# Kernel tuning notes

Hardware: AMD Instinct MI355X
Metric: run time of the kernel (lower is better)

## Reference

```python
import jax, jax.numpy as jnp
import numpy as np

N_SEGMENT = 8   # frames per clip (init arg n_segment)
P = 4           # patch_size (init arg)
EPS = 1e-5      # torch F.layer_norm default eps


def setup_inputs() -> dict:
    key = jax.random.key(0)
    # (b*t, c, h, w) = (16*8, 256, 28, 28)
    x = jax.random.normal(key, (128, 256, 28, 28), dtype=jnp.float32)
    return {"x": x}


def _layer_norm(x):
    # F.layer_norm over last dim, no affine params
    m = jnp.mean(x, axis=-1, keepdims=True)
    v = jnp.var(x, axis=-1, keepdims=True)
    return (x - m) * jax.lax.rsqrt(v + EPS)


def _self_attention(x):
    # q = k = v = x; scores = softmax(q k^T / sqrt(E)); out = scores @ v
    e = x.shape[-1]
    scores = jnp.einsum('bqe,bke->bqk', x, x) * (1.0 / float(np.sqrt(e)))
    scores = jax.nn.softmax(scores, axis=-1)
    return jnp.einsum('bqk,bke->bqe', scores, x)


def reference(x):
    t, p = N_SEGMENT, P
    bt, c, h, w = x.shape
    b = bt // t
    ph, pw = h // p, w // p
    e = p * p * c  # patch embedding dim = 4096

    # rearrange '(b t) c (ph p1) (pw p2) -> (b ph pw) t (p1 p2 c)'
    y = x.reshape(b, t, c, ph, p, pw, p)
    y = y.transpose(0, 3, 5, 1, 4, 6, 2).reshape(b * ph * pw, t, e)

    # temporal: layernorm + shift-left-diff + self-attention + residual
    xn = _layer_norm(y)
    xn = jnp.concatenate([xn[:, 1:], jnp.zeros_like(xn[:, :1])], axis=1) - xn
    y = _self_attention(xn) + y

    # rearrange '(b ph pw) t e -> (b t) (ph pw) e'
    y = y.reshape(b, ph, pw, t, e).transpose(0, 3, 1, 2, 4).reshape(b * t, ph * pw, e)

    # spatial: layernorm + self-attention + residual
    xn = _layer_norm(y)
    y = _self_attention(xn) + y

    # rearrange '(b t) (ph pw) (p1 p2 c) -> (b t) c (ph p1) (pw p2)'
    y = y.reshape(b, t, ph, pw, p, p, c)
    y = y.transpose(0, 1, 6, 2, 4, 3, 5).reshape(bt, c, h, w)
    return y
```

## Files before the change

### kernel.cpp

```cpp
#include <hip/hip_runtime.h>


#define IDX36(a,b) ((((a)*8)+(b))-((((a)*((a)+1)))/2))

typedef __attribute__((ext_vector_type(8)))  short bf16x8;
typedef __attribute__((ext_vector_type(16))) float f32x16;

__device__ __forceinline__ float wsum64(float v){
  #pragma unroll
  for (int off=32; off; off>>=1) v += __shfl_xor(v, off);
  return v;
}
__device__ __forceinline__ float wsum32(float v){
  #pragma unroll
  for (int off=16; off; off>>=1) v += __shfl_xor(v, off);
  return v;
}
__device__ __forceinline__ unsigned int rne_bf16(float f){
  unsigned int b = __float_as_uint(f);
  return (b + 0x7FFFu + ((b>>16)&1u)) >> 16;
}

__global__ __launch_bounds__(256) void k_t1(const float* __restrict__ x, float* __restrict__ wsG){
  const int bx = blockIdx.x;
  const int b = bx / 112;
  const int ph = (bx % 112) / 16;
  const int slice = bx & 15;
  const int c0 = slice * 16;
  const int tid = threadIdx.x;

  __shared__ float lds[8*16*116];
  const float4* x4 = reinterpret_cast<const float4*>(x);

  #pragma unroll
  for (int t=0;t<8;t++){
    const int base = ((b*8+t)*256 + c0)*196 + ph*28;
    {
      const int f = tid, c = f/28, m = f%28;
      *reinterpret_cast<float4*>(&lds[(t*16+c)*116 + m*4]) = x4[base + c*196 + m];
    }
    if (tid < 192){
      const int f = 256+tid, c = f/28, m = f%28;
      *reinterpret_cast<float4*>(&lds[(t*16+c)*116 + m*4]) = x4[base + c*196 + m];
    }
  }
  __syncthreads();

  const int pw   = tid >> 5;
  const int slot = tid & 31;
  const int c    = slot >> 1;
  const int p1b  = (slot & 1) * 2;

  float v[8][8];
  #pragma unroll
  for (int t=0;t<8;t++){
    const float* p = &lds[(t*16+c)*116 + p1b*28 + pw*4];
    const float4 a  = *reinterpret_cast<const float4*>(p);
    const float4 b2 = *reinterpret_cast<const float4*>(p + 28);
    v[t][0]=a.x;  v[t][1]=a.y;  v[t][2]=a.z;  v[t][3]=a.w;
    v[t][4]=b2.x; v[t][5]=b2.y; v[t][6]=b2.z; v[t][7]=b2.w;
  }

  float Au[36], sm[8];
  #pragma unroll
  for (int a2=0;a2<8;a2++){
    float s0 = 0.f;
    #pragma unroll
    for (int e=0;e<8;e++) s0 += v[a2][e];
    sm[a2] = s0;
    #pragma unroll
    for (int b2=a2;b2<8;b2++){
      float s = 0.f;
      #pragma unroll
      for (int e=0;e<8;e++) s += v[a2][e]*v[b2][e];
      Au[IDX36(a2,b2)] = s;
    }
  }
  #pragma unroll
  for (int i=0;i<36;i++) Au[i] = wsum32(Au[i]);
  #pragma unroll
  for (int t=0;t<8;t++) sm[t] = wsum32(sm[t]);

  if (slot == 0 && pw < 7){
    const int base = ((b*49 + ph*7 + pw)*16 + slice)*44;
    #pragma unroll
    for (int i=0;i<36;i++) wsG[base+i] = Au[i];
    #pragma unroll
    for (int t=0;t<8;t++)  wsG[base+36+t] = sm[t];
  }
}

__global__ __launch_bounds__(64) void k_t2(const float* __restrict__ wsG, float* __restrict__ wsWt){
  const int seq = blockIdx.x;
  const int lane = threadIdx.x;
  __shared__ float red[44];
  if (lane < 44){
    float a = 0.f;
    #pragma unroll
    for (int s=0;s<16;s++) a += wsG[(seq*16+s)*44 + lane];
    red[lane] = a;
  }
  __syncthreads();
  if (lane < 8){
    const int i = lane;
    float Ar[36], mean[8], rstd[8];
    #pragma unroll
    for (int k=0;k<36;k++) Ar[k] = red[k];
    #pragma unroll
    for (int t=0;t<8;t++){
      const float sv = red[36+t];
      mean[t] = sv * (1.f/4096.f);
      const float var = Ar[IDX36(t,t)] * (1.f/4096.f) - mean[t]*mean[t];
      rstd[t] = rsqrtf(var + 1e-5f);
    }
    #define GV(a,b) ((((a)<8)&&((b)<8)) ? (rstd[(a)]*rstd[(b)]*(Ar[((a)<=(b))?IDX36((a),(b)):IDX36((b),(a))] - 4096.f*mean[(a)]*mean[(b)])) : 0.f)
    float l[8]; float mx = -1e30f;
    #pragma unroll
    for (int j=0;j<8;j++){
      const float sij = GV(i+1,j+1) - GV(i+1,j) - GV(i,j+1) + GV(i,j);
      l[j] = sij * (1.f/64.f);
      mx = fmaxf(mx, l[j]);
    }
    float ss = 0.f;
    #pragma unroll
    for (int j=0;j<8;j++){ l[j] = __expf(l[j]-mx); ss += l[j]; }
    const float inv = 1.f/ss;
    float cc = 0.f;
    #pragma unroll
    for (int k2=0;k2<8;k2++){
      const float q = (((k2>=1)? l[k2-1] : 0.f) - l[k2]) * inv;
      const float wv2 = q * rstd[k2];
      wsWt[seq*72 + i*8 + k2] = wv2;
      cc -= wv2 * mean[k2];
    }
    wsWt[seq*72 + 64 + i] = cc;
    #undef GV
  }
}

__global__ __launch_bounds__(256) void k_t3(const float* __restrict__ x, const float* __restrict__ wsWt,
                                            unsigned short* __restrict__ y1u){
  const int bx = blockIdx.x;
  const int b = bx / 112;
  const int ph = (bx % 112) / 16;
  const int slice = bx & 15;
  const int c0 = slice * 16;
  const int tid = threadIdx.x;

  __shared__ float Wl[7][72];
  for (int idx=tid; idx<504; idx+=256)
    Wl[idx/72][idx%72] = wsWt[(b*49 + ph*7 + idx/72)*72 + idx%72];
  __syncthreads();

  const float4* x4 = reinterpret_cast<const float4*>(x);

  #pragma unroll
  for (int fi=0; fi<2; fi++){
    const int f = fi*256 + tid;
    if (f < 448){
      const int c = f/28, m = f%28, pw = m%7, p1 = m/7;
      float4 v[8];
      #pragma unroll
      for (int t=0;t<8;t++) v[t] = x4[((b*8+t)*256 + c0+c)*196 + ph*28 + m];
      const float* W = Wl[pw];
      const int pp = ph*7 + pw;
      #pragma unroll
      for (int i=0;i<8;i++){
        const float ci = W[64+i];
        float4 o;
        o.x = v[i].x + ci; o.y = v[i].y + ci; o.z = v[i].z + ci; o.w = v[i].w + ci;
        #pragma unroll
        for (int j=0;j<8;j++){
          const float w = W[i*8+j];
          o.x += w*v[j].x; o.y += w*v[j].y; o.z += w*v[j].z; o.w += w*v[j].w;
        }
        const unsigned int h0=rne_bf16(o.x), h1=rne_bf16(o.y), h2=rne_bf16(o.z), h3=rne_bf16(o.w);
        const unsigned int l0=rne_bf16(o.x-__uint_as_float(h0<<16));
        const unsigned int l1=rne_bf16(o.y-__uint_as_float(h1<<16));
        const unsigned int l2=rne_bf16(o.z-__uint_as_float(h2<<16));
        const unsigned int l3=rne_bf16(o.w-__uint_as_float(h3<<16));
        const size_t ybase = (size_t)((b*8+i)*49 + pp)*8192 + (c0+c)*16 + p1*4;
        *reinterpret_cast<uint2*>(&y1u[ybase])        = make_uint2(h0|(h1<<16), h2|(h3<<16));
        *reinterpret_cast<uint2*>(&y1u[ybase + 4096]) = make_uint2(l0|(l1<<16), l2|(l3<<16));
      }
    }
  }
}

__global__ __launch_bounds__(256,3) void k_s1(const unsigned short* __restrict__ y1u, float* __restrict__ wsA){
  const int bt = blockIdx.x >> 2;
  const int slice = blockIdx.x & 3;
  const int tid = threadIdx.x;
  const int wave = tid >> 6, lane = tid & 63;

  __shared__ unsigned short Ah[64*136];
  __shared__ float red[64*52];
  for (int i=tid; i<64*52; i+=256) red[i] = 0.f;

  for (int idx=tid; idx<15*128; idx+=256){
    const int rr = 49 + idx/128, cc = idx%128;
    Ah[rr*136 + cc] = (rr==49) ? (unsigned short)0x3F80 : (unsigned short)0;
  }

  f32x16 acc00, acc01, acc11;
  #pragma unroll
  for (int i=0;i<16;i++){ acc00[i]=0.f; acc01[i]=0.f; acc11[i]=0.f; }

  const int r0 = lane & 31;
  const int koff = (lane >> 5) * 8;
  const int lrow = tid >> 4;
  const int lq   = tid & 15;

#define ISSUE(pf, ch) { \
  _Pragma("unroll") \
  for (int p=0;p<4;p++){ \
    const int row = p*16 + lrow; \
    pf[p] = make_uint4(0u,0u,0u,0u); \
    if (row < 49) pf[p] = *reinterpret_cast<const uint4*>(&y1u[(size_t)(bt*49+row)*8192 + slice*1024 + (ch)*128 + lq*8]); } }

#define CW(pf) { \
  _Pragma("unroll") \
  for (int p=0;p<4;p++){ \
    const int row = p*16 + lrow; \
    if (row < 49) *reinterpret_cast<uint4*>(&Ah[row*136 + lq*8]) = pf[p]; } }

#define MF() { \
  _Pragma("unroll") \
  for (int kk=0;kk<2;kk++){ \
    const int kw = (wave + kk*4)*16; \
    const bf16x8 f0 = *reinterpret_cast<const bf16x8*>(&Ah[ r0     *136 + kw + koff]); \
    const bf16x8 f1 = *reinterpret_cast<const bf16x8*>(&Ah[(32+r0)*136 + kw + koff]); \
    acc00 = __builtin_amdgcn_mfma_f32_32x32x16_bf16(f0, f0, acc00, 0,0,0); \
    acc01 = __builtin_amdgcn_mfma_f32_32x32x16_bf16(f0, f1, acc01, 0,0,0); \
    acc11 = __builtin_amdgcn_mfma_f32_32x32x16_bf16(f1, f1, acc11, 0,0,0); } }

  uint4 pfA[4], pfB[4];
  ISSUE(pfA, 0);
  #pragma unroll
  for (int ch=0; ch<8; ch+=2){
    if (ch+1<8) ISSUE(pfB, ch+1);
    __syncthreads();
    CW(pfA);
    __syncthreads();
    MF();
    if (ch+2<8) ISSUE(pfA, ch+2);
    __syncthreads();
    CW(pfB);
    __syncthreads();
    MF();
  }
  __syncthreads();

  const int ccol = lane & 31;
  const int rbase = 4*(lane>>5);
  #pragma unroll
  for (int q2=0;q2<16;q2++){
    const int rr = (q2&3) + 8*(q2>>2) + rbase;
    atomicAdd(&red[ rr    *52 + ccol     ], acc00[q2]);
    atomicAdd(&red[ rr    *52 + 32 + ccol], acc01[q2]);
    atomicAdd(&red[(rr+32)*52 + 32 + ccol], acc11[q2]);
  }
  __syncthreads();
  float* wp = wsA + blockIdx.x * 2500;
  for (int idx=tid; idx<2500; idx+=256){
    const int i2 = idx/50, j2 = idx%50;
    wp[idx] = (i2>=32 && j2<32) ? red[j2*52+i2] : red[i2*52+j2];
  }
#undef ISSUE
#undef CW
#undef MF
}

__global__ __launch_bounds__(256) void k_s2(const float* __restrict__ wsA, float* __restrict__ wsWT, float* __restrict__ wsC){
  const int bt = blockIdx.x;
  const int tid = threadIdx.x;
  __shared__ float A[2500];
  __shared__ float m[49], r[49];
  for (int idx=tid; idx<2548; idx+=256) wsWT[bt*2548+idx] = 0.f;
  for (int idx=tid; idx<2500; idx+=256){
    float v = 0.f;
    #pragma unroll
    for (int sl=0; sl<4; sl++) v += wsA[(bt*4+sl)*2500 + idx];
    A[idx] = v;
  }
  __syncthreads();
  if (tid < 49){
    const float mm = A[49*50+tid] * (1.f/4096.f);
    const float var = A[tid*50+tid] * (1.f/4096.f) - mm*mm;
    m[tid]=mm; r[tid]=rsqrtf(var+1e-5f);
  }
  __syncthreads();
  const int wv = tid>>6, lane = tid&63;
  for (int i=wv; i<49; i+=4){
    const float ri = r[i], mi = m[i];
    float rv=0.f, mv=0.f, L=-1e30f;
    if (lane < 49){
      rv = r[lane]; mv = m[lane];
      L = ri*rv*(A[i*50+lane] - 4096.f*mi*mv) * (1.f/64.f);
    }
    float mx = L;
    #pragma unroll
    for (int off=32; off; off>>=1) mx = fmaxf(mx, __shfl_xor(mx, off));
    const float p = (lane<49) ? __expf(L-mx) : 0.f;
    const float ss = wsum64(p);
    const float Wv = (p/ss)*rv;
    if (lane < 49) wsWT[bt*2548 + lane*52 + i] = Wv + ((lane==i) ? 1.f : 0.f);
    const float cp = wsum64(-Wv*mv);
    if (lane == 0) wsC[bt*49+i] = cp;
  }
}

__global__ __launch_bounds__(256,2) void k_s3(const unsigned short* __restrict__ y1u, const float* __restrict__ wsWT,
                                              const float* __restrict__ wsC, float* __restrict__ out){
  const int bt = blockIdx.x >> 2;
  const int chunk = blockIdx.x & 3;
  const int tid = threadIdx.x;
  const int wave = tid >> 6, lane = tid & 63;

  __shared__ unsigned short Wh[64*68], Wlo[64*68];
  __shared__ unsigned short Yh[4][32*68], Ylo[4][32*68];

  for (int idx=tid; idx<64*64; idx+=256){
    const int i = idx>>6, j = idx&63;
    float v = 0.f;
    if (i < 49){
      if (j < 49)       v = wsWT[bt*2548 + j*52 + i];
      else if (j == 49) v = wsC[bt*49 + i];
    }
    const unsigned int u = __float_as_uint(v);
    const float lo = v - __uint_as_float(u & 0xFFFF0000u);
    Wh [i*68+j] = (unsigned short)(u>>16);
    Wlo[i*68+j] = (unsigned short)rne_bf16(lo);
  }
  unsigned short* yh = &Yh[wave][0];
  unsigned short* yl = &Ylo[wave][0];
  for (int idx=lane; idx<32*16; idx+=64){
    const int e = idx>>4, jj = idx&15;
    if (jj > 0){
      yh[e*68 + 48 + jj] = (jj==1) ? 0x3F80 : 0;
      yl[e*68 + 48 + jj] = 0;
    }
  }
  __syncthreads();

  const int r0 = lane & 31;
  const int koff = (lane >> 5) * 8;
  bf16x8 A0h[4], A0l[4], A1h[4], A1l[4];
  #pragma unroll
  for (int kk=0;kk<4;kk++){
    const int off = kk*16 + koff;
    A0h[kk] = *reinterpret_cast<const bf16x8*>(&Wh [ r0     *68 + off]);
    A0l[kk] = *reinterpret_cast<const bf16x8*>(&Wlo[ r0     *68 + off]);
    A1h[kk] = *reinterpret_cast<const bf16x8*>(&Wh [(32+r0)*68 + off]);
    A1l[kk] = *reinterpret_cast<const bf16x8*>(&Wlo[(32+r0)*68 + off]);
  }

  const unsigned short* ybu = y1u + (size_t)bt*49*8192;
  float* ob_base = out + bt*200704;

#define S3_LOAD(pf, t) { \
  const int ecol0 = chunk*1024 + ((t)*4+wave)*32; \
  _Pragma("unroll") \
  for (int p=0;p<7;p++){ \
    const int idx = p*64 + lane; const int j = idx>>3; const int sub = idx&7; \
    pf[p] = make_uint4(0u,0u,0u,0u); \
    if (j < 49) pf[p] = *reinterpret_cast<const uint4*>(&ybu[(size_t)j*8192 + (sub>>2)*4096 + ecol0 + (sub&3)*8]); } }

#define S3_WRITE(pf) { \
  _Pragma("unroll") \
  for (int p=0;p<7;p++){ \
    const int idx = p*64 + lane; const int j = idx>>3; const int sub = idx&7; \
    if (j < 49){ \
      unsigned short* dst = (sub>>2) ? yl : yh; \
      const int e0 = (sub&3)*8; \
      const unsigned int uu[4] = {pf[p].x, pf[p].y, pf[p].z, pf[p].w}; \
      _Pragma("unroll") \
      for (int s=0;s<4;s++){ \
        dst[(e0 + s*2    )*68 + j] = (unsigned short)(uu[s] & 0xFFFFu); \
        dst[(e0 + s*2 + 1)*68 + j] = (unsigned short)(uu[s] >> 16); } } } }

  uint4 pf[7];
  S3_LOAD(pf, 0);
  S3_WRITE(pf);

  #pragma unroll
  for (int t=0;t<8;t++){
    if (t < 7) S3_LOAD(pf, t+1);

    f32x16 acc0, acc1;
    #pragma unroll
    for (int i=0;i<16;i++){ acc0[i]=0.f; acc1[i]=0.f; }

    #pragma unroll
    for (int kk=0;kk<4;kk++){
      const int off = kk*16 + koff;
      const bf16x8 Bh = *reinterpret_cast<const bf16x8*>(&yh[r0*68 + off]);
      const bf16x8 Bl = *reinterpret_cast<const bf16x8*>(&yl[r0*68 + off]);
      acc0 = __builtin_amdgcn_mfma_f32_32x32x16_bf16(A0h[kk], Bh, acc0, 0,0,0);
      acc0 = __builtin_amdgcn_mfma_f32_32x32x16_bf16(A0h[kk], Bl, acc0, 0,0,0);
      acc0 = __builtin_amdgcn_mfma_f32_32x32x16_bf16(A0l[kk], Bh, acc0, 0,0,0);
      acc1 = __builtin_amdgcn_mfma_f32_32x32x16_bf16(A1h[kk], Bh, acc1, 0,0,0);
      acc1 = __builtin_amdgcn_mfma_f32_32x32x16_bf16(A1h[kk], Bl, acc1, 0,0,0);
      acc1 = __builtin_amdgcn_mfma_f32_32x32x16_bf16(A1l[kk], Bh, acc1, 0,0,0);
    }

    {
      const int ecol = chunk*1024 + (t*4+wave)*32 + r0;
      const int c  = ecol >> 4;
      const int p1 = (ecol >> 2) & 3;
      const int p2 = ecol & 3;
      float* ob = ob_base + c*784 + p1*28 + p2;
      const int rbase = 4*(lane>>5);
      #pragma unroll
      for (int q=0;q<16;q++){
        const int i0 = (q&3) + 8*(q>>2) + rbase;
        ob[(i0/7)*112 + (i0%7)*4] = acc0[q];
        const int i1 = 32 + i0;
        if (i1 < 49) ob[(i1/7)*112 + (i1%7)*4] = acc1[q];
      }
    }

    if (t < 7) S3_WRITE(pf);
  }
#undef S3_LOAD
#undef S3_WRITE
}

extern "C" void kernel_launch(void* const* d_in, const int* in_sizes, int n_in,
                              void* d_out, int out_size, void* d_ws, size_t ws_size,
                              hipStream_t stream) {
  const float* x = (const float*)d_in[0];
  float* out = (float*)d_out;
  float* ws  = (float*)d_ws;
  unsigned short* y1u = (unsigned short*)ws;
  float* wsA  = ws + 25690112;
  float* wsWT = wsA + 512*2500;
  float* wsC  = wsWT + 128*2548;
  float* wsG  = wsA;
  float* wsWt = wsA + 551936;
  hipLaunchKernelGGL(k_t1, dim3(1792), dim3(256), 0, stream, x, wsG);
  hipLaunchKernelGGL(k_t2, dim3(784),  dim3(64),  0, stream, wsG, wsWt);
  hipLaunchKernelGGL(k_t3, dim3(1792), dim3(256), 0, stream, x, wsWt, y1u);
  hipLaunchKernelGGL(k_s1, dim3(512),  dim3(256), 0, stream, y1u, wsA);
  hipLaunchKernelGGL(k_s2, dim3(128),  dim3(256), 0, stream, wsA, wsWT, wsC);
  hipLaunchKernelGGL(k_s3, dim3(512),  dim3(256), 0, stream, y1u, wsWT, wsC, out);
}
```

Measured before the change: 199.9 us.

## Fuse softmax-weight kernels into their consumer kernels to cut launches

Removes the two small kernels that turned the Gram reductions into attention weights and recomputes that step inside the consuming kernels. k_t3 now sums the 16 partial Gram slices and builds the 8x8 temporal weights in shared memory itself. k_s3 sums the spatial Gram partials and builds the 49x49 softmax matrix directly as split-bf16 in shared memory, reusing the Y staging buffer through a union. This removes two launches and a global round trip for the weights. In exchange, the reduction and softmax work is repeated in every block that needs it: k_t3 redoes it once per channel slice and k_s3 once per chunk.

```diff
diff --git a/kernel.cpp b/kernel.cpp
--- a/kernel.cpp
+++ b/kernel.cpp
@@ -90,55 +90,7 @@
   }
 }
 
-__global__ __launch_bounds__(64) void k_t2(const float* __restrict__ wsG, float* __restrict__ wsWt){
-  const int seq = blockIdx.x;
-  const int lane = threadIdx.x;
-  __shared__ float red[44];
-  if (lane < 44){
-    float a = 0.f;
-    #pragma unroll
-    for (int s=0;s<16;s++) a += wsG[(seq*16+s)*44 + lane];
-    red[lane] = a;
-  }
-  __syncthreads();
-  if (lane < 8){
-    const int i = lane;
-    float Ar[36], mean[8], rstd[8];
-    #pragma unroll
-    for (int k=0;k<36;k++) Ar[k] = red[k];
-    #pragma unroll
-    for (int t=0;t<8;t++){
-      const float sv = red[36+t];
-      mean[t] = sv * (1.f/4096.f);
-      const float var = Ar[IDX36(t,t)] * (1.f/4096.f) - mean[t]*mean[t];
-      rstd[t] = rsqrtf(var + 1e-5f);
-    }
-    #define GV(a,b) ((((a)<8)&&((b)<8)) ? (rstd[(a)]*rstd[(b)]*(Ar[((a)<=(b))?IDX36((a),(b)):IDX36((b),(a))] - 4096.f*mean[(a)]*mean[(b)])) : 0.f)
-    float l[8]; float mx = -1e30f;
-    #pragma unroll
-    for (int j=0;j<8;j++){
-      const float sij = GV(i+1,j+1) - GV(i+1,j) - GV(i,j+1) + GV(i,j);
-      l[j] = sij * (1.f/64.f);
-      mx = fmaxf(mx, l[j]);
-    }
-    float ss = 0.f;
-    #pragma unroll
-    for (int j=0;j<8;j++){ l[j] = __expf(l[j]-mx); ss += l[j]; }
-    const float inv = 1.f/ss;
-    float cc = 0.f;
-    #pragma unroll
-    for (int k2=0;k2<8;k2++){
-      const float q = (((k2>=1)? l[k2-1] : 0.f) - l[k2]) * inv;
-      const float wv2 = q * rstd[k2];
-      wsWt[seq*72 + i*8 + k2] = wv2;
-      cc -= wv2 * mean[k2];
-    }
-    wsWt[seq*72 + 64 + i] = cc;
-    #undef GV
-  }
-}
-
-__global__ __launch_bounds__(256) void k_t3(const float* __restrict__ x, const float* __restrict__ wsWt,
+__global__ __launch_bounds__(256) void k_t3(const float* __restrict__ x, const float* __restrict__ wsG,
                                             unsigned short* __restrict__ y1u){
   const int bx = blockIdx.x;
   const int b = bx / 112;
@@ -148,8 +100,54 @@
   const int tid = threadIdx.x;
 
   __shared__ float Wl[7][72];
-  for (int idx=tid; idx<504; idx+=256)
-    Wl[idx/72][idx%72] = wsWt[(b*49 + ph*7 + idx/72)*72 + idx%72];
+  __shared__ float redG[7][44];
+
+  for (int idx=tid; idx<308; idx+=256){
+    const int g = idx/44, k = idx%44;
+    float a = 0.f;
+    #pragma unroll
+    for (int s=0;s<16;s++) a += wsG[((b*49 + ph*7 + g)*16 + s)*44 + k];
+    redG[g][k] = a;
+  }
+  __syncthreads();
+
+  {
+    const int g = tid >> 5, i = tid & 31;
+    if (g < 7 && i < 8){
+      float Ar[36], mean[8], rstd[8];
+      #pragma unroll
+      for (int k=0;k<36;k++) Ar[k] = redG[g][k];
+      #pragma unroll
+      for (int t=0;t<8;t++){
+        const float sv = redG[g][36+t];
+        mean[t] = sv * (1.f/4096.f);
+        const float var = Ar[IDX36(t,t)] * (1.f/4096.f) - mean[t]*mean[t];
+        rstd[t] = rsqrtf(var + 1e-5f);
+      }
+      #define GV(a,b) ((((a)<8)&&((b)<8)) ? (rstd[(a)]*rstd[(b)]*(Ar[((a)<=(b))?IDX36((a),(b)):IDX36((b),(a))] - 4096.f*mean[(a)]*mean[(b)])) : 0.f)
+      float l[8]; float mx = -1e30f;
+      #pragma unroll
+      for (int j=0;j<8;j++){
+        const float sij = GV(i+1,j+1) - GV(i+1,j) - GV(i,j+1) + GV(i,j);
+        l[j] = sij * (1.f/64.f);
+        mx = fmaxf(mx, l[j]);
+      }
+      float ss = 0.f;
+      #pragma unroll
+      for (int j=0;j<8;j++){ l[j] = __expf(l[j]-mx); ss += l[j]; }
+      const float inv = 1.f/ss;
+      float cc = 0.f;
+      #pragma unroll
+      for (int k2=0;k2<8;k2++){
+        const float q = (((k2>=1)? l[k2-1] : 0.f) - l[k2]) * inv;
+        const float wv2 = q * rstd[k2];
+        Wl[g][i*8+k2] = wv2;
+        cc -= wv2 * mean[k2];
+      }
+      Wl[g][64+i] = cc;
+      #undef GV
+    }
+  }
   __syncthreads();
 
   const float4* x4 = reinterpret_cast<const float4*>(x);
@@ -271,32 +269,40 @@
 #undef MF
 }
 
-__global__ __launch_bounds__(256) void k_s2(const float* __restrict__ wsA, float* __restrict__ wsWT, float* __restrict__ wsC){
-  const int bt = blockIdx.x;
+__global__ __launch_bounds__(256,2) void k_s3(const unsigned short* __restrict__ y1u, const float* __restrict__ wsA,
+                                              float* __restrict__ out){
+  const int bt = blockIdx.x >> 2;
+  const int chunk = blockIdx.x & 3;
   const int tid = threadIdx.x;
-  __shared__ float A[2500];
-  __shared__ float m[49], r[49];
-  for (int idx=tid; idx<2548; idx+=256) wsWT[bt*2548+idx] = 0.f;
+  const int wave = tid >> 6, lane = tid & 63;
+
+  __shared__ unsigned short Wh[64*68], Wlo[64*68];
+  __shared__ union SM {
+    float A[2500];
+    struct { unsigned short Yh[4][2176]; unsigned short Ylo[4][2176]; } y;
+  } um;
+  __shared__ float ms[49], rs[49];
+
+  for (int idx=tid; idx<64*68; idx+=256){ Wh[idx]=0; Wlo[idx]=0; }
   for (int idx=tid; idx<2500; idx+=256){
     float v = 0.f;
     #pragma unroll
     for (int sl=0; sl<4; sl++) v += wsA[(bt*4+sl)*2500 + idx];
-    A[idx] = v;
+    um.A[idx] = v;
   }
   __syncthreads();
   if (tid < 49){
-    const float mm = A[49*50+tid] * (1.f/4096.f);
-    const float var = A[tid*50+tid] * (1.f/4096.f) - mm*mm;
-    m[tid]=mm; r[tid]=rsqrtf(var+1e-5f);
-  }
-  __syncthreads();
-  const int wv = tid>>6, lane = tid&63;
-  for (int i=wv; i<49; i+=4){
-    const float ri = r[i], mi = m[i];
+    const float mm = um.A[49*50+tid] * (1.f/4096.f);
+    const float var = um.A[tid*50+tid] * (1.f/4096.f) - mm*mm;
+    ms[tid]=mm; rs[tid]=rsqrtf(var+1e-5f);
+  }
+  __syncthreads();
+  for (int i=wave; i<49; i+=4){
+    const float ri = rs[i], mi = ms[i];
     float rv=0.f, mv=0.f, L=-1e30f;
     if (lane < 49){
-      rv = r[lane]; mv = m[lane];
-      L = ri*rv*(A[i*50+lane] - 4096.f*mi*mv) * (1.f/64.f);
+      rv = rs[lane]; mv = ms[lane];
+      L = ri*rv*(um.A[i*50+lane] - 4096.f*mi*mv) * (1.f/64.f);
     }
     float mx = L;
     #pragma unroll
@@ -304,36 +310,23 @@
     const float p = (lane<49) ? __expf(L-mx) : 0.f;
     const float ss = wsum64(p);
     const float Wv = (p/ss)*rv;
-    if (lane < 49) wsWT[bt*2548 + lane*52 + i] = Wv + ((lane==i) ? 1.f : 0.f);
+    if (lane < 49){
+      const float v = Wv + ((lane==i) ? 1.f : 0.f);
+      const unsigned int u = __float_as_uint(v);
+      Wh [i*68+lane] = (unsigned short)(u>>16);
+      Wlo[i*68+lane] = (unsigned short)rne_bf16(v - __uint_as_float(u & 0xFFFF0000u));
+    }
     const float cp = wsum64(-Wv*mv);
-    if (lane == 0) wsC[bt*49+i] = cp;
-  }
-}
-
-__global__ __launch_bounds__(256,2) void k_s3(const unsigned short* __restrict__ y1u, const float* __restrict__ wsWT,
-                                              const float* __restrict__ wsC, float* __restrict__ out){
-  const int bt = blockIdx.x >> 2;
-  const int chunk = blockIdx.x & 3;
-  const int tid = threadIdx.x;
-  const int wave = tid >> 6, lane = tid & 63;
-
-  __shared__ unsigned short Wh[64*68], Wlo[64*68];
-  __shared__ unsigned short Yh[4][32*68], Ylo[4][32*68];
-
-  for (int idx=tid; idx<64*64; idx+=256){
-    const int i = idx>>6, j = idx&63;
-    float v = 0.f;
-    if (i < 49){
-      if (j < 49)       v = wsWT[bt*2548 + j*52 + i];
-      else if (j == 49) v = wsC[bt*49 + i];
-    }
-    const unsigned int u = __float_as_uint(v);
-    const float lo = v - __uint_as_float(u & 0xFFFF0000u);
-    Wh [i*68+j] = (unsigned short)(u>>16);
-    Wlo[i*68+j] = (unsigned short)rne_bf16(lo);
-  }
-  unsigned short* yh = &Yh[wave][0];
-  unsigned short* yl = &Ylo[wave][0];
+    if (lane == 0){
+      const unsigned int u = __float_as_uint(cp);
+      Wh [i*68+49] = (unsigned short)(u>>16);
+      Wlo[i*68+49] = (unsigned short)rne_bf16(cp - __uint_as_float(u & 0xFFFF0000u));
+    }
+  }
+  __syncthreads();
+
+  unsigned short* yh = &um.y.Yh[wave][0];
+  unsigned short* yl = &um.y.Ylo[wave][0];
   for (int idx=lane; idx<32*16; idx+=64){
     const int e = idx>>4, jj = idx&15;
     if (jj > 0){
@@ -341,7 +334,6 @@
       yl[e*68 + 48 + jj] = 0;
     }
   }
-  __syncthreads();
 
   const int r0 = lane & 31;
   const int koff = (lane >> 5) * 8;
@@ -434,14 +426,9 @@
   float* ws  = (float*)d_ws;
   unsigned short* y1u = (unsigned short*)ws;
   float* wsA  = ws + 25690112;
-  float* wsWT = wsA + 512*2500;
-  float* wsC  = wsWT + 128*2548;
   float* wsG  = wsA;
-  float* wsWt = wsA + 551936;
   hipLaunchKernelGGL(k_t1, dim3(1792), dim3(256), 0, stream, x, wsG);
-  hipLaunchKernelGGL(k_t2, dim3(784),  dim3(64),  0, stream, wsG, wsWt);
-  hipLaunchKernelGGL(k_t3, dim3(1792), dim3(256), 0, stream, x, wsWt, y1u);
+  hipLaunchKernelGGL(k_t3, dim3(1792), dim3(256), 0, stream, x, wsG, y1u);
   hipLaunchKernelGGL(k_s1, dim3(512),  dim3(256), 0, stream, y1u, wsA);
-  hipLaunchKernelGGL(k_s2, dim3(128),  dim3(256), 0, stream, wsA, wsWT, wsC);
-  hipLaunchKernelGGL(k_s3, dim3(512),  dim3(256), 0, stream, y1u, wsWT, wsC, out);
-}
+  hipLaunchKernelGGL(k_s3, dim3(512),  dim3(256), 0, stream, y1u, wsA, out);
+}
```

Result: slower. 233.8 us (+17.0%).

## Replace MFMA split-bf16 spatial output GEMM with scalar FP32 FMA kernel

Applied to the files above, without the earlier changes.

The final spatial kernel k_s3 no longer uses bf16 hi/lo MFMA with LDS transposes. Each thread now computes two embedding columns for 25 output rows, using scalar FMAs over the 49 source rows. The hi/lo y values are summed to fp32 on load, and weights are read through wave-uniform loads. The grid grows to 2048 blocks, with the output rows split into two halves. This removes the LDS staging, the transposed shared-memory writes and the three-pass MFMA work, and adds occupancy, at the cost of scalar FLOPs and y being reread by both halves.

```diff
diff --git a/kernel.cpp b/kernel.cpp
--- a/kernel.cpp
+++ b/kernel.cpp
@@ -310,120 +310,49 @@
   }
 }
 
-__global__ __launch_bounds__(256,2) void k_s3(const unsigned short* __restrict__ y1u, const float* __restrict__ wsWT,
+__global__ __launch_bounds__(256,4) void k_s3(const unsigned short* __restrict__ y1u, const float* __restrict__ wsWT,
                                               const float* __restrict__ wsC, float* __restrict__ out){
-  const int bt = blockIdx.x >> 2;
-  const int chunk = blockIdx.x & 3;
-  const int tid = threadIdx.x;
-  const int wave = tid >> 6, lane = tid & 63;
-
-  __shared__ unsigned short Wh[64*68], Wlo[64*68];
-  __shared__ unsigned short Yh[4][32*68], Ylo[4][32*68];
-
-  for (int idx=tid; idx<64*64; idx+=256){
-    const int i = idx>>6, j = idx&63;
-    float v = 0.f;
+  const int bt = blockIdx.x >> 4;
+  const int chunk = (blockIdx.x >> 1) & 7;
+  const int half = blockIdx.x & 1;
+  const int tid = threadIdx.x;
+  const int i0 = half ? 25 : 0;
+
+  const int e0 = chunk*512 + tid*2;
+  const unsigned short* yb = y1u + (size_t)bt*49*8192;
+  const float* Wb = wsWT + bt*2548 + i0;
+  const float* cb = wsC + bt*49;
+
+  float2 acc[25];
+  #pragma unroll
+  for (int r=0;r<25;r++){ acc[r].x=0.f; acc[r].y=0.f; }
+
+  for (int j=0;j<49;++j){
+    const unsigned int hu = *reinterpret_cast<const unsigned int*>(&yb[(size_t)j*8192 + e0]);
+    const unsigned int lu = *reinterpret_cast<const unsigned int*>(&yb[(size_t)j*8192 + 4096 + e0]);
+    float2 v;
+    v.x = __uint_as_float(hu<<16) + __uint_as_float(lu<<16);
+    v.y = __uint_as_float(hu & 0xFFFF0000u) + __uint_as_float(lu & 0xFFFF0000u);
+    const float* wr = Wb + __builtin_amdgcn_readfirstlane(j*52);
+    #pragma unroll
+    for (int r=0;r<25;r++){
+      const float w = wr[r];
+      acc[r].x += w*v.x; acc[r].y += w*v.y;
+    }
+  }
+
+  const int c  = e0 >> 4;
+  const int p1 = (e0 >> 2) & 3;
+  const int p2 = e0 & 3;
+  float* ob = out + bt*200704 + c*784 + p1*28 + p2;
+  #pragma unroll
+  for (int r=0;r<25;r++){
+    const int i = i0 + r;
     if (i < 49){
-      if (j < 49)       v = wsWT[bt*2548 + j*52 + i];
-      else if (j == 49) v = wsC[bt*49 + i];
-    }
-    const unsigned int u = __float_as_uint(v);
-    const float lo = v - __uint_as_float(u & 0xFFFF0000u);
-    Wh [i*68+j] = (unsigned short)(u>>16);
-    Wlo[i*68+j] = (unsigned short)rne_bf16(lo);
-  }
-  unsigned short* yh = &Yh[wave][0];
-  unsigned short* yl = &Ylo[wave][0];
-  for (int idx=lane; idx<32*16; idx+=64){
-    const int e = idx>>4, jj = idx&15;
-    if (jj > 0){
-      yh[e*68 + 48 + jj] = (jj==1) ? 0x3F80 : 0;
-      yl[e*68 + 48 + jj] = 0;
-    }
-  }
-  __syncthreads();
-
-  const int r0 = lane & 31;
-  const int koff = (lane >> 5) * 8;
-  bf16x8 A0h[4], A0l[4], A1h[4], A1l[4];
-  #pragma unroll
-  for (int kk=0;kk<4;kk++){
-    const int off = kk*16 + koff;
-    A0h[kk] = *reinterpret_cast<const bf16x8*>(&Wh [ r0     *68 + off]);
-    A0l[kk] = *reinterpret_cast<const bf16x8*>(&Wlo[ r0     *68 + off]);
-    A1h[kk] = *reinterpret_cast<const bf16x8*>(&Wh [(32+r0)*68 + off]);
-    A1l[kk] = *reinterpret_cast<const bf16x8*>(&Wlo[(32+r0)*68 + off]);
-  }
-
-  const unsigned short* ybu = y1u + (size_t)bt*49*8192;
-  float* ob_base = out + bt*200704;
-
-#define S3_LOAD(pf, t) { \
-  const int ecol0 = chunk*1024 + ((t)*4+wave)*32; \
-  _Pragma("unroll") \
-  for (int p=0;p<7;p++){ \
-    const int idx = p*64 + lane; const int j = idx>>3; const int sub = idx&7; \
-    pf[p] = make_uint4(0u,0u,0u,0u); \
-    if (j < 49) pf[p] = *reinterpret_cast<const uint4*>(&ybu[(size_t)j*8192 + (sub>>2)*4096 + ecol0 + (sub&3)*8]); } }
-
-#define S3_WRITE(pf) { \
-  _Pragma("unroll") \
-  for (int p=0;p<7;p++){ \
-    const int idx = p*64 + lane; const int j = idx>>3; const int sub = idx&7; \
-    if (j < 49){ \
-      unsigned short* dst = (sub>>2) ? yl : yh; \
-      const int e0 = (sub&3)*8; \
-      const unsigned int uu[4] = {pf[p].x, pf[p].y, pf[p].z, pf[p].w}; \
-      _Pragma("unroll") \
-      for (int s=0;s<4;s++){ \
-        dst[(e0 + s*2    )*68 + j] = (unsigned short)(uu[s] & 0xFFFFu); \
-        dst[(e0 + s*2 + 1)*68 + j] = (unsigned short)(uu[s] >> 16); } } } }
-
-  uint4 pf[7];
-  S3_LOAD(pf, 0);
-  S3_WRITE(pf);
-
-  #pragma unroll
-  for (int t=0;t<8;t++){
-    if (t < 7) S3_LOAD(pf, t+1);
-
-    f32x16 acc0, acc1;
-    #pragma unroll
-    for (int i=0;i<16;i++){ acc0[i]=0.f; acc1[i]=0.f; }
-
-    #pragma unroll
-    for (int kk=0;kk<4;kk++){
-      const int off = kk*16 + koff;
-      const bf16x8 Bh = *reinterpret_cast<const bf16x8*>(&yh[r0*68 + off]);
-      const bf16x8 Bl = *reinterpret_cast<const bf16x8*>(&yl[r0*68 + off]);
-      acc0 = __builtin_amdgcn_mfma_f32_32x32x16_bf16(A0h[kk], Bh, acc0, 0,0,0);
-      acc0 = __builtin_amdgcn_mfma_f32_32x32x16_bf16(A0h[kk], Bl, acc0, 0,0,0);
-      acc0 = __builtin_amdgcn_mfma_f32_32x32x16_bf16(A0l[kk], Bh, acc0, 0,0,0);
-      acc1 = __builtin_amdgcn_mfma_f32_32x32x16_bf16(A1h[kk], Bh, acc1, 0,0,0);
-      acc1 = __builtin_amdgcn_mfma_f32_32x32x16_bf16(A1h[kk], Bl, acc1, 0,0,0);
-      acc1 = __builtin_amdgcn_mfma_f32_32x32x16_bf16(A1l[kk], Bh, acc1, 0,0,0);
-    }
-
-    {
-      const int ecol = chunk*1024 + (t*4+wave)*32 + r0;
-      const int c  = ecol >> 4;
-      const int p1 = (ecol >> 2) & 3;
-      const int p2 = ecol & 3;
-      float* ob = ob_base + c*784 + p1*28 + p2;
-      const int rbase = 4*(lane>>5);
-      #pragma unroll
-      for (int q=0;q<16;q++){
-        const int i0 = (q&3) + 8*(q>>2) + rbase;
-        ob[(i0/7)*112 + (i0%7)*4] = acc0[q];
-        const int i1 = 32 + i0;
-        if (i1 < 49) ob[(i1/7)*112 + (i1%7)*4] = acc1[q];
-      }
-    }
-
-    if (t < 7) S3_WRITE(pf);
-  }
-#undef S3_LOAD
-#undef S3_WRITE
+      const float ci = cb[i];
+      *reinterpret_cast<float2*>(ob + (i/7)*112 + (i%7)*4) = make_float2(acc[r].x + ci, acc[r].y + ci);
+    }
+  }
 }
 
 extern "C" void kernel_launch(void* const* d_in, const int* in_sizes, int n_in,
@@ -443,5 +372,5 @@
   hipLaunchKernelGGL(k_t3, dim3(1792), dim3(256), 0, stream, x, wsWt, y1u);
   hipLaunchKernelGGL(k_s1, dim3(512),  dim3(256), 0, stream, y1u, wsA);
   hipLaunchKernelGGL(k_s2, dim3(128),  dim3(256), 0, stream, wsA, wsWT, wsC);
-  hipLaunchKernelGGL(k_s3, dim3(512),  dim3(256), 0, stream, y1u, wsWT, wsC, out);
-}
+  hipLaunchKernelGGL(k_s3, dim3(2048), dim3(256), 0, stream, y1u, wsWT, wsC, out);
+}
```

Result: slower. 212.0 us (+6.1%).

## Load k_s3 B fragments directly from global memory, drop LDS staging, double grid

Applied to the files above, without the earlier changes.

The spatial output kernel no longer stages y1 tiles through shared memory with software prefetch. Each lane now gathers its bf16 B-fragment elements straight from global memory with strided 2-byte loads. The grid doubles to 1024 blocks, each covering 512 columns. This removes the LDS transpose writes and a large shared-memory footprint, which may raise occupancy. In exchange it issues many uncoalesced scalar global loads and loses the load/compute overlap.

```diff
diff --git a/kernel.cpp b/kernel.cpp
--- a/kernel.cpp
+++ b/kernel.cpp
@@ -312,14 +312,12 @@
 
 __global__ __launch_bounds__(256,2) void k_s3(const unsigned short* __restrict__ y1u, const float* __restrict__ wsWT,
                                               const float* __restrict__ wsC, float* __restrict__ out){
-  const int bt = blockIdx.x >> 2;
-  const int chunk = blockIdx.x & 3;
+  const int bt = blockIdx.x >> 3;
+  const int chunk = blockIdx.x & 7;
   const int tid = threadIdx.x;
   const int wave = tid >> 6, lane = tid & 63;
 
   __shared__ unsigned short Wh[64*68], Wlo[64*68];
-  __shared__ unsigned short Yh[4][32*68], Ylo[4][32*68];
-
   for (int idx=tid; idx<64*64; idx+=256){
     const int i = idx>>6, j = idx&63;
     float v = 0.f;
@@ -328,18 +326,8 @@
       else if (j == 49) v = wsC[bt*49 + i];
     }
     const unsigned int u = __float_as_uint(v);
-    const float lo = v - __uint_as_float(u & 0xFFFF0000u);
     Wh [i*68+j] = (unsigned short)(u>>16);
-    Wlo[i*68+j] = (unsigned short)rne_bf16(lo);
-  }
-  unsigned short* yh = &Yh[wave][0];
-  unsigned short* yl = &Ylo[wave][0];
-  for (int idx=lane; idx<32*16; idx+=64){
-    const int e = idx>>4, jj = idx&15;
-    if (jj > 0){
-      yh[e*68 + 48 + jj] = (jj==1) ? 0x3F80 : 0;
-      yl[e*68 + 48 + jj] = 0;
-    }
+    Wlo[i*68+j] = (unsigned short)rne_bf16(v - __uint_as_float(u & 0xFFFF0000u));
   }
   __syncthreads();
 
@@ -357,35 +345,12 @@
 
   const unsigned short* ybu = y1u + (size_t)bt*49*8192;
   float* ob_base = out + bt*200704;
-
-#define S3_LOAD(pf, t) { \
-  const int ecol0 = chunk*1024 + ((t)*4+wave)*32; \
-  _Pragma("unroll") \
-  for (int p=0;p<7;p++){ \
-    const int idx = p*64 + lane; const int j = idx>>3; const int sub = idx&7; \
-    pf[p] = make_uint4(0u,0u,0u,0u); \
-    if (j < 49) pf[p] = *reinterpret_cast<const uint4*>(&ybu[(size_t)j*8192 + (sub>>2)*4096 + ecol0 + (sub&3)*8]); } }
-
-#define S3_WRITE(pf) { \
-  _Pragma("unroll") \
-  for (int p=0;p<7;p++){ \
-    const int idx = p*64 + lane; const int j = idx>>3; const int sub = idx&7; \
-    if (j < 49){ \
-      unsigned short* dst = (sub>>2) ? yl : yh; \
-      const int e0 = (sub&3)*8; \
-      const unsigned int uu[4] = {pf[p].x, pf[p].y, pf[p].z, pf[p].w}; \
-      _Pragma("unroll") \
-      for (int s=0;s<4;s++){ \
-        dst[(e0 + s*2    )*68 + j] = (unsigned short)(uu[s] & 0xFFFFu); \
-        dst[(e0 + s*2 + 1)*68 + j] = (unsigned short)(uu[s] >> 16); } } } }
-
-  uint4 pf[7];
-  S3_LOAD(pf, 0);
-  S3_WRITE(pf);
-
-  #pragma unroll
-  for (int t=0;t<8;t++){
-    if (t < 7) S3_LOAD(pf, t+1);
+  const bool lo32 = (lane < 32);
+
+  #pragma unroll
+  for (int tt=0; tt<4; tt++){
+    const int ecol = chunk*512 + (wave*4+tt)*32 + r0;
+    const unsigned short* pb = ybu + koff*8192 + ecol;
 
     f32x16 acc0, acc1;
     #pragma unroll
@@ -393,9 +358,21 @@
 
     #pragma unroll
     for (int kk=0;kk<4;kk++){
-      const int off = kk*16 + koff;
-      const bf16x8 Bh = *reinterpret_cast<const bf16x8*>(&yh[r0*68 + off]);
-      const bf16x8 Bl = *reinterpret_cast<const bf16x8*>(&yl[r0*68 + off]);
+      bf16x8 Bh, Bl;
+      if (kk < 3){
+        #pragma unroll
+        for (int s=0;s<8;s++){
+          Bh[s] = (short)pb[(kk*16+s)*8192];
+          Bl[s] = (short)pb[(kk*16+s)*8192 + 4096];
+        }
+      } else {
+        const unsigned short h48 = lo32 ? pb[48*8192]        : (unsigned short)0;
+        const unsigned short l48 = lo32 ? pb[48*8192 + 4096] : (unsigned short)0;
+        Bh[0] = (short)h48;                    Bl[0] = (short)l48;
+        Bh[1] = lo32 ? (short)0x3F80 : (short)0; Bl[1] = 0;
+        #pragma unroll
+        for (int s=2;s<8;s++){ Bh[s]=0; Bl[s]=0; }
+      }
       acc0 = __builtin_amdgcn_mfma_f32_32x32x16_bf16(A0h[kk], Bh, acc0, 0,0,0);
       acc0 = __builtin_amdgcn_mfma_f32_32x32x16_bf16(A0h[kk], Bl, acc0, 0,0,0);
       acc0 = __builtin_amdgcn_mfma_f32_32x32x16_bf16(A0l[kk], Bh, acc0, 0,0,0);
@@ -404,26 +381,19 @@
       acc1 = __builtin_amdgcn_mfma_f32_32x32x16_bf16(A1l[kk], Bh, acc1, 0,0,0);
     }
 
-    {
-      const int ecol = chunk*1024 + (t*4+wave)*32 + r0;
-      const int c  = ecol >> 4;
-      const int p1 = (ecol >> 2) & 3;
-      const int p2 = ecol & 3;
-      float* ob = ob_base + c*784 + p1*28 + p2;
-      const int rbase = 4*(lane>>5);
-      #pragma unroll
-      for (int q=0;q<16;q++){
-        const int i0 = (q&3) + 8*(q>>2) + rbase;
-        ob[(i0/7)*112 + (i0%7)*4] = acc0[q];
-        const int i1 = 32 + i0;
-        if (i1 < 49) ob[(i1/7)*112 + (i1%7)*4] = acc1[q];
-      }
-    }
-
-    if (t < 7) S3_WRITE(pf);
-  }
-#undef S3_LOAD
-#undef S3_WRITE
+    const int c  = ecol >> 4;
+    const int p1 = (ecol >> 2) & 3;
+    const int p2 = ecol & 3;
+    float* ob = ob_base + c*784 + p1*28 + p2;
+    const int rbase = 4*(lane>>5);
+    #pragma unroll
+    for (int q=0;q<16;q++){
+      const int i0 = (q&3) + 8*(q>>2) + rbase;
+      ob[(i0/7)*112 + (i0%7)*4] = acc0[q];
+      const int i1 = 32 + i0;
+      if (i1 < 49) ob[(i1/7)*112 + (i1%7)*4] = acc1[q];
+    }
+  }
 }
 
 extern "C" void kernel_launch(void* const* d_in, const int* in_sizes, int n_in,
@@ -443,5 +413,5 @@
   hipLaunchKernelGGL(k_t3, dim3(1792), dim3(256), 0, stream, x, wsWt, y1u);
   hipLaunchKernelGGL(k_s1, dim3(512),  dim3(256), 0, stream, y1u, wsA);
   hipLaunchKernelGGL(k_s2, dim3(128),  dim3(256), 0, stream, wsA, wsWT, wsC);
-  hipLaunchKernelGGL(k_s3, dim3(512),  dim3(256), 0, stream, y1u, wsWT, wsC, out);
-}
+  hipLaunchKernelGGL(k_s3, dim3(1024), dim3(256), 0, stream, y1u, wsWT, wsC, out);
+}
```

Measured after the change: 211.4 us. 1.06x slower.
